# Performance work log

Measured on AMD Instinct MI355X. Metric: run time of the kernel, lower is better.

## Reference

```python
import jax, jax.numpy as jnp
import numpy as np

THRESHOLD = 1.0
SLOPE = 25.0  # snntorch surrogate.fast_sigmoid default

@jax.custom_vjp
def spike_fn(x):
    # heaviside forward, fast_sigmoid surrogate backward
    return (x > 0).astype(x.dtype)

def _spike_fwd(x):
    return spike_fn(x), x

def _spike_bwd(x, g):
    return (g / (SLOPE * jnp.abs(x) + 1.0) ** 2,)

spike_fn.defvjp(_spike_fwd, _spike_bwd)


def setup_inputs() -> dict:
    key = jax.random.key(0)
    ks = jax.random.split(key, 8)
    B, D_IN, H0, H1 = 16384, 512, 1024, 512
    def linear_params(kw, kb, fan_in, fan_out):
        bound = 1.0 / np.sqrt(fan_in)
        w = jax.random.uniform(kw, (fan_out, fan_in), jnp.float32, -bound, bound)
        b = jax.random.uniform(kb, (fan_out,), jnp.float32, -bound, bound)
        return w, b
    w1, b1 = linear_params(ks[0], ks[1], D_IN, H0)
    w2, b2 = linear_params(ks[2], ks[3], H0, H1)
    w3, b3 = linear_params(ks[4], ks[5], H1, 1)
    data = jax.random.normal(ks[6], (B, D_IN), jnp.float32)
    return {"data": data, "w1": w1, "b1": b1, "w2": w2, "b2": b2,
            "w3": w3, "b3": b3, "time_steps": 8}


def reference(data, w1, b1, w2, b2, w3, b3, time_steps):
    # Effective betas: snntorch clamps beta to [0,1]. lif1 beta = units0 (=1024) -> 1.0 (source bug, replicated).
    beta1 = jnp.float32(1.0)
    beta2 = jnp.float32(0.95)
    # data is constant across time, so fc1 output is step-invariant
    cur1 = data @ w1.T + b1                      # [B, H0]
    B, H0 = cur1.shape
    H1 = w2.shape[0]
    mem1_0 = jnp.zeros((B, H0), cur1.dtype)
    mem2_0 = jnp.zeros((B, H1), cur1.dtype)

    def step(carry, _):
        mem1, mem2 = carry
        # snntorch Leaky (reset_mechanism='subtract'): reset detected on OLD mem, detached
        reset1 = jax.lax.stop_gradient((mem1 > THRESHOLD).astype(mem1.dtype))
        mem1 = beta1 * mem1 + cur1 - reset1 * THRESHOLD
        spk1 = spike_fn(mem1 - THRESHOLD)
        cur2 = spk1 @ w2.T + b2                  # [B, H1]
        reset2 = jax.lax.stop_gradient((mem2 > THRESHOLD).astype(mem2.dtype))
        mem2 = beta2 * mem2 + cur2 - reset2 * THRESHOLD
        spk2 = spike_fn(mem2 - THRESHOLD)
        cur3 = spk2 @ w3.T + b3                  # [B, 1]
        return (mem1, mem2), cur3

    _, cur3_seq = jax.lax.scan(step, (mem1_0, mem2_0), None, length=time_steps)
    return jnp.mean(cur3_seq, axis=0)            # [B, 1]
```

## Files before the change

### kernel.cpp

```cpp
#include <hip/hip_runtime.h>
#include <hip/hip_bf16.h>
#include <cstdint>
#include <cstddef>


#define NB 16384
#define DIN 512
#define NH0 1024
#define NH1 512

typedef float f32x4 __attribute__((ext_vector_type(4)));
typedef short bf16x8 __attribute__((ext_vector_type(8)));

#define WS_PAT   0u
#define WS_W2H   19922944u
#define WS_W2M   20971520u
#define WS_W2L   22020096u

__device__ inline uint16_t f2bf(float f) {
    __hip_bfloat16 h = __float2bfloat16(f);
    return *reinterpret_cast<uint16_t*>(&h);
}
__device__ inline float bf2f(uint16_t u) {
    __hip_bfloat16 h = *reinterpret_cast<__hip_bfloat16*>(&u);
    return __bfloat162float(h);
}

__global__ void init_out_kernel(float* __restrict__ out,
                                const float* __restrict__ b3, int n) {
    int i = blockIdx.x * blockDim.x + threadIdx.x;
    if (i < n) out[i] = b3[0];
}

__global__ __launch_bounds__(256) void split3_kernel(
    const float* __restrict__ src, uint16_t* __restrict__ h,
    uint16_t* __restrict__ m, uint16_t* __restrict__ l, int n)
{
    int i = (blockIdx.x * 256 + threadIdx.x) * 4;
    if (i >= n) return;
    float4 f = *(const float4*)(src + i);
    float fv[4] = {f.x, f.y, f.z, f.w};
    uint32_t hw[2], mw[2], lw[2];
    #pragma unroll
    for (int g = 0; g < 2; ++g) {
        uint16_t hh[2], mm[2], ll[2];
        #pragma unroll
        for (int e = 0; e < 2; ++e) {
            float a = fv[2 * g + e];
            uint16_t h0 = f2bf(a);
            float d = __fsub_rn(a, bf2f(h0));
            uint16_t m0 = f2bf(d);
            float e2 = __fsub_rn(d, bf2f(m0));
            uint16_t l0 = f2bf(e2);
            hh[e] = h0; mm[e] = m0; ll[e] = l0;
        }
        hw[g] = (uint32_t)hh[0] | ((uint32_t)hh[1] << 16);
        mw[g] = (uint32_t)mm[0] | ((uint32_t)mm[1] << 16);
        lw[g] = (uint32_t)ll[0] | ((uint32_t)ll[1] << 16);
    }
    *(uint2*)(h + i) = make_uint2(hw[0], hw[1]);
    *(uint2*)(m + i) = make_uint2(mw[0], mw[1]);
    *(uint2*)(l + i) = make_uint2(lw[0], lw[1]);
}

__global__ __launch_bounds__(512, 4) void gemm1_spike_kernel(
    const float* __restrict__ data, const float* __restrict__ w1,
    const float* __restrict__ b1, uint8_t* __restrict__ pat)
{
    __shared__ float As[128][68];
    __shared__ float Bs[128][68];
    const int tid = threadIdx.x;
    const int tx = tid & 31;
    const int ty = tid >> 5;
    const int i0 = blockIdx.x * 128, n0 = blockIdx.y * 128;

    float acc[8][4] = {};

    for (int kb = 0; kb < DIN; kb += 64) {
        #pragma unroll
        for (int rep = 0; rep < 4; ++rep) {
            int idx = tid + rep * 512;
            int row = idx >> 4, c4 = (idx & 15) * 4;
            *(float4*)(&As[row][c4]) =
                *(const float4*)(data + (size_t)(i0 + row) * DIN + kb + c4);
            *(float4*)(&Bs[row][c4]) =
                *(const float4*)(w1 + (size_t)(n0 + row) * DIN + kb + c4);
        }
        __syncthreads();
        #pragma unroll 2
        for (int k4 = 0; k4 < 16; ++k4) {
            float4 a4[8], b4[4];
            #pragma unroll
            for (int ii = 0; ii < 8; ++ii)
                a4[ii] = *(const float4*)(&As[ty + ii * 16][k4 * 4]);
            #pragma unroll
            for (int nn = 0; nn < 4; ++nn)
                b4[nn] = *(const float4*)(&Bs[tx + nn * 32][k4 * 4]);
            #pragma unroll
            for (int ii = 0; ii < 8; ++ii) {
                #pragma unroll
                for (int nn = 0; nn < 4; ++nn) {
                    acc[ii][nn] = fmaf(a4[ii].x, b4[nn].x, acc[ii][nn]);
                    acc[ii][nn] = fmaf(a4[ii].y, b4[nn].y, acc[ii][nn]);
                    acc[ii][nn] = fmaf(a4[ii].z, b4[nn].z, acc[ii][nn]);
                    acc[ii][nn] = fmaf(a4[ii].w, b4[nn].w, acc[ii][nn]);
                }
            }
        }
        __syncthreads();
    }

    #pragma unroll
    for (int ii = 0; ii < 8; ++ii) {
        const int i = i0 + ty + ii * 16;
        #pragma unroll
        for (int nn = 0; nn < 4; ++nn) {
            const int n = n0 + tx + nn * 32;
            float x = __fadd_rn(acc[ii][nn], b1[n]);
            float mem = 0.0f;
            unsigned p = 0;
            #pragma unroll
            for (int t = 0; t < 8; ++t) {
                bool reset = mem > 1.0f;
                float tmp = __fadd_rn(mem, x);
                mem = reset ? __fsub_rn(tmp, 1.0f) : tmp;
                p |= (mem > 1.0f ? 1u : 0u) << t;
            }
            pat[(size_t)(n >> 6) * (NB * 64) + (size_t)i * 64 + (n & 63)] = (uint8_t)p;
        }
    }
}

__global__ __launch_bounds__(256, 2) void gemm2_mfma_kernel(
    const uint8_t* __restrict__ pat,
    const uint16_t* __restrict__ w2h, const uint16_t* __restrict__ w2m,
    const uint16_t* __restrict__ w2l,
    const float* __restrict__ b2, const float* __restrict__ w3,
    float* __restrict__ out)
{
    __shared__ __align__(16) uint16_t Bhi[2][64][72];
    __shared__ __align__(16) uint16_t Bmd[2][64][72];
    __shared__ __align__(16) uint16_t Blo[2][64][72];
    __shared__ __align__(16) uint8_t  Ap[2][64][80];

    const int tid  = threadIdx.x;
    const int lane = tid & 63;
    const int wv   = tid >> 6;
    const int lr   = lane & 15;
    const int lg   = lane >> 4;
    const int i0   = blockIdx.x * 64, n0 = blockIdx.y * 64;

    f32x4 acc[8][4];
    #pragma unroll
    for (int t = 0; t < 8; ++t)
        #pragma unroll
        for (int nf = 0; nf < 4; ++nf)
            acc[t][nf] = (f32x4)(0.0f);

    const int srow = tid >> 2;
    const int scol = (tid & 3) * 16;
    const size_t wbase = (size_t)(n0 + srow) * NH0 + scol;
    const size_t pbase = (size_t)i0 * 64 + (size_t)tid * 16;

    uint4 rh0, rh1, rm0, rm1, rl0, rl1, rp;

    {
        const uint16_t* s1 = w2h + wbase;
        const uint16_t* s2 = w2m + wbase;
        const uint16_t* s3 = w2l + wbase;
        rh0 = *(const uint4*)(s1); rh1 = *(const uint4*)(s1 + 8);
        rm0 = *(const uint4*)(s2); rm1 = *(const uint4*)(s2 + 8);
        rl0 = *(const uint4*)(s3); rl1 = *(const uint4*)(s3 + 8);
        rp  = *(const uint4*)(pat + pbase);
        *(uint4*)(&Bhi[0][srow][scol])     = rh0;
        *(uint4*)(&Bhi[0][srow][scol + 8]) = rh1;
        *(uint4*)(&Bmd[0][srow][scol])     = rm0;
        *(uint4*)(&Bmd[0][srow][scol + 8]) = rm1;
        *(uint4*)(&Blo[0][srow][scol])     = rl0;
        *(uint4*)(&Blo[0][srow][scol + 8]) = rl1;
        *(uint4*)(&Ap[0][srow][scol])      = rp;
    }

    int cur = 0;
    for (int kbi = 0; kbi < 16; ++kbi) {
        __syncthreads();
        if (kbi < 15) {
            const int kb = (kbi + 1) * 64;
            const uint16_t* s1 = w2h + wbase + kb;
            const uint16_t* s2 = w2m + wbase + kb;
            const uint16_t* s3 = w2l + wbase + kb;
            rh0 = *(const uint4*)(s1); rh1 = *(const uint4*)(s1 + 8);
            rm0 = *(const uint4*)(s2); rm1 = *(const uint4*)(s2 + 8);
            rl0 = *(const uint4*)(s3); rl1 = *(const uint4*)(s3 + 8);
            rp  = *(const uint4*)(pat + (size_t)(kbi + 1) * (NB * 64) + pbase);
        }

        #pragma unroll
        for (int s = 0; s < 2; ++s) {
            const int k0 = s * 32;
            bf16x8 bh[4], bm[4], bl[4];
            #pragma unroll
            for (int nf = 0; nf < 4; ++nf) {
                const int col = nf * 16 + lr;
                bh[nf] = *(const bf16x8*)(&Bhi[cur][col][k0 + lg * 8]);
                bm[nf] = *(const bf16x8*)(&Bmd[cur][col][k0 + lg * 8]);
                bl[nf] = *(const bf16x8*)(&Blo[cur][col][k0 + lg * 8]);
            }
            const uint2 p8 = *(const uint2*)(&Ap[cur][wv * 16 + lr][k0 + lg * 8]);
            #pragma unroll
            for (int t = 0; t < 8; ++t) {
                uint32_t y0 = (p8.x >> t) & 0x01010101u;
                uint32_t y1 = (p8.y >> t) & 0x01010101u;
                uint32_t s0 = __builtin_amdgcn_perm(0u, y0, 0x01010000u) | 0x02000200u;
                uint32_t s1x = __builtin_amdgcn_perm(0u, y0, 0x03030202u) | 0x02000200u;
                uint32_t s2x = __builtin_amdgcn_perm(0u, y1, 0x01010000u) | 0x02000200u;
                uint32_t s3x = __builtin_amdgcn_perm(0u, y1, 0x03030202u) | 0x02000200u;
                union { uint4 u; bf16x8 v; } af;
                af.u = make_uint4(__builtin_amdgcn_perm(0u, 0x3F008000u, s0),
                                  __builtin_amdgcn_perm(0u, 0x3F008000u, s1x),
                                  __builtin_amdgcn_perm(0u, 0x3F008000u, s2x),
                                  __builtin_amdgcn_perm(0u, 0x3F008000u, s3x));
                #pragma unroll
                for (int nf = 0; nf < 4; ++nf) {
                    acc[t][nf] = __builtin_amdgcn_mfma_f32_16x16x32_bf16(
                        af.v, bh[nf], acc[t][nf], 0, 0, 0);
                    acc[t][nf] = __builtin_amdgcn_mfma_f32_16x16x32_bf16(
                        af.v, bm[nf], acc[t][nf], 0, 0, 0);
                    acc[t][nf] = __builtin_amdgcn_mfma_f32_16x16x32_bf16(
                        af.v, bl[nf], acc[t][nf], 0, 0, 0);
                }
            }
        }

        if (kbi < 15) {
            const int nb = cur ^ 1;
            *(uint4*)(&Bhi[nb][srow][scol])     = rh0;
            *(uint4*)(&Bhi[nb][srow][scol + 8]) = rh1;
            *(uint4*)(&Bmd[nb][srow][scol])     = rm0;
            *(uint4*)(&Bmd[nb][srow][scol + 8]) = rm1;
            *(uint4*)(&Blo[nb][srow][scol])     = rl0;
            *(uint4*)(&Blo[nb][srow][scol + 8]) = rl1;
            *(uint4*)(&Ap[nb][srow][scol])      = rp;
        }
        cur ^= 1;
    }

    float rowsum[4] = {0.0f, 0.0f, 0.0f, 0.0f};
    #pragma unroll
    for (int nf = 0; nf < 4; ++nf) {
        const int n = n0 + nf * 16 + lr;
        const float b2n = b2[n];
        const float w3n = w3[n];
        #pragma unroll
        for (int r = 0; r < 4; ++r) {
            float mem = 0.0f;
            int pc = 0;
            #pragma unroll
            for (int t = 0; t < 8; ++t) {
                bool reset = mem > 1.0f;
                float x   = __fadd_rn(acc[t][nf][r], b2n);
                float tmp = __fadd_rn(__fmul_rn(0.95f, mem), x);
                mem = reset ? __fsub_rn(tmp, 1.0f) : tmp;
                pc += (mem > 1.0f) ? 1 : 0;
            }
            rowsum[r] = fmaf(w3n, (float)pc, rowsum[r]);
        }
    }
    #pragma unroll
    for (int r = 0; r < 4; ++r) {
        float s = rowsum[r];
        s += __shfl_xor(s, 1);
        s += __shfl_xor(s, 2);
        s += __shfl_xor(s, 4);
        s += __shfl_xor(s, 8);
        if (lr == 0)
            atomicAdd(&out[i0 + wv * 16 + lg * 4 + r], 0.125f * s);
    }
}

extern "C" void kernel_launch(void* const* d_in, const int* in_sizes, int n_in,
                              void* d_out, int out_size, void* d_ws, size_t ws_size,
                              hipStream_t stream) {
    const float* data = (const float*)d_in[0];
    const float* w1   = (const float*)d_in[1];
    const float* b1   = (const float*)d_in[2];
    const float* w2   = (const float*)d_in[3];
    const float* b2   = (const float*)d_in[4];
    const float* w3   = (const float*)d_in[5];
    const float* b3   = (const float*)d_in[6];
    float* out = (float*)d_out;

    char* ws = (char*)d_ws;
    uint8_t*  pat = (uint8_t*)(ws + WS_PAT);
    uint16_t* w2h = (uint16_t*)(ws + WS_W2H);
    uint16_t* w2m = (uint16_t*)(ws + WS_W2M);
    uint16_t* w2l = (uint16_t*)(ws + WS_W2L);

    init_out_kernel<<<(NB + 255) / 256, 256, 0, stream>>>(out, b3, NB);
    split3_kernel<<<(NH1 * NH0 / 4 + 255) / 256, 256, 0, stream>>>(w2, w2h, w2m, w2l, NH1 * NH0);
    gemm1_spike_kernel<<<dim3(NB / 128, NH0 / 128), 512, 0, stream>>>(data, w1, b1, pat);
    gemm2_mfma_kernel<<<dim3(NB / 64, NH1 / 64), 256, 0, stream>>>(pat, w2h, w2m, w2l, b2, w3, out);
}
```

Baseline: 563.1 us.

## Split time steps across two wave groups in gemm2 to halve accumulators

Doubles the gemm2 block to 512 threads: each group of four waves computes four of the eight time steps, so each wave holds half as many accumulators and register pressure drops (launch bounds now 512,3). The first group's accumulators are exchanged through a 64KB shared buffer so the LIF recurrence can run sequentially in one group. Shared-memory staging is flattened into a raw buffer, and each thread loads half as much per tile. The cost is duplicated B-fragment LDS reads and an extra shared-memory pass at the end, and the 64KB of LDS per block may cap residency.

```diff
diff --git a/kernel.cpp b/kernel.cpp
--- a/kernel.cpp
+++ b/kernel.cpp
@@ -131,54 +131,53 @@
     }
 }
 
-__global__ __launch_bounds__(256, 2) void gemm2_mfma_kernel(
+__global__ __launch_bounds__(512, 3) void gemm2_mfma_kernel(
     const uint8_t* __restrict__ pat,
     const uint16_t* __restrict__ w2h, const uint16_t* __restrict__ w2m,
     const uint16_t* __restrict__ w2l,
     const float* __restrict__ b2, const float* __restrict__ w3,
     float* __restrict__ out)
 {
-    __shared__ __align__(16) uint16_t Bhi[2][64][72];
-    __shared__ __align__(16) uint16_t Bmd[2][64][72];
-    __shared__ __align__(16) uint16_t Blo[2][64][72];
-    __shared__ __align__(16) uint8_t  Ap[2][64][80];
+    __shared__ __align__(16) uint8_t lds_raw[65536];
+    uint16_t* Bh_ = (uint16_t*)lds_raw;
+    uint16_t* Bm_ = (uint16_t*)(lds_raw + 18432);
+    uint16_t* Bl_ = (uint16_t*)(lds_raw + 36864);
+    uint8_t*  Ap_ = lds_raw + 55296;
 
     const int tid  = threadIdx.x;
     const int lane = tid & 63;
     const int wv   = tid >> 6;
+    const int tg   = wv >> 2;
+    const int ig   = wv & 3;
     const int lr   = lane & 15;
     const int lg   = lane >> 4;
     const int i0   = blockIdx.x * 64, n0 = blockIdx.y * 64;
 
-    f32x4 acc[8][4];
+    f32x4 acc[4][4];
     #pragma unroll
-    for (int t = 0; t < 8; ++t)
+    for (int tl = 0; tl < 4; ++tl)
         #pragma unroll
         for (int nf = 0; nf < 4; ++nf)
-            acc[t][nf] = (f32x4)(0.0f);
-
-    const int srow = tid >> 2;
-    const int scol = (tid & 3) * 16;
-    const size_t wbase = (size_t)(n0 + srow) * NH0 + scol;
+            acc[tl][nf] = (f32x4)(0.0f);
+
+    const int srow = tid >> 3;
+    const int sc8  = (tid & 7) * 8;
+    const size_t wbase = (size_t)(n0 + srow) * NH0 + sc8;
     const size_t pbase = (size_t)i0 * 64 + (size_t)tid * 16;
 
-    uint4 rh0, rh1, rm0, rm1, rl0, rl1, rp;
+    uint4 rh, rm, rl, rp;
 
     {
-        const uint16_t* s1 = w2h + wbase;
-        const uint16_t* s2 = w2m + wbase;
-        const uint16_t* s3 = w2l + wbase;
-        rh0 = *(const uint4*)(s1); rh1 = *(const uint4*)(s1 + 8);
-        rm0 = *(const uint4*)(s2); rm1 = *(const uint4*)(s2 + 8);
-        rl0 = *(const uint4*)(s3); rl1 = *(const uint4*)(s3 + 8);
-        rp  = *(const uint4*)(pat + pbase);
-        *(uint4*)(&Bhi[0][srow][scol])     = rh0;
-        *(uint4*)(&Bhi[0][srow][scol + 8]) = rh1;
-        *(uint4*)(&Bmd[0][srow][scol])     = rm0;
-        *(uint4*)(&Bmd[0][srow][scol + 8]) = rm1;
-        *(uint4*)(&Blo[0][srow][scol])     = rl0;
-        *(uint4*)(&Blo[0][srow][scol + 8]) = rl1;
-        *(uint4*)(&Ap[0][srow][scol])      = rp;
+        rh = *(const uint4*)(w2h + wbase);
+        rm = *(const uint4*)(w2m + wbase);
+        rl = *(const uint4*)(w2l + wbase);
+        *(uint4*)(Bh_ + srow * 72 + sc8) = rh;
+        *(uint4*)(Bm_ + srow * 72 + sc8) = rm;
+        *(uint4*)(Bl_ + srow * 72 + sc8) = rl;
+        if (tid < 256) {
+            rp = *(const uint4*)(pat + pbase);
+            *(uint4*)(Ap_ + (tid >> 2) * 80 + (tid & 3) * 16) = rp;
+        }
     }
 
     int cur = 0;
@@ -186,13 +185,11 @@
         __syncthreads();
         if (kbi < 15) {
             const int kb = (kbi + 1) * 64;
-            const uint16_t* s1 = w2h + wbase + kb;
-            const uint16_t* s2 = w2m + wbase + kb;
-            const uint16_t* s3 = w2l + wbase + kb;
-            rh0 = *(const uint4*)(s1); rh1 = *(const uint4*)(s1 + 8);
-            rm0 = *(const uint4*)(s2); rm1 = *(const uint4*)(s2 + 8);
-            rl0 = *(const uint4*)(s3); rl1 = *(const uint4*)(s3 + 8);
-            rp  = *(const uint4*)(pat + (size_t)(kbi + 1) * (NB * 64) + pbase);
+            rh = *(const uint4*)(w2h + wbase + kb);
+            rm = *(const uint4*)(w2m + wbase + kb);
+            rl = *(const uint4*)(w2l + wbase + kb);
+            if (tid < 256)
+                rp = *(const uint4*)(pat + (size_t)(kbi + 1) * (NB * 64) + pbase);
         }
 
         #pragma unroll
@@ -202,13 +199,15 @@
             #pragma unroll
             for (int nf = 0; nf < 4; ++nf) {
                 const int col = nf * 16 + lr;
-                bh[nf] = *(const bf16x8*)(&Bhi[cur][col][k0 + lg * 8]);
-                bm[nf] = *(const bf16x8*)(&Bmd[cur][col][k0 + lg * 8]);
-                bl[nf] = *(const bf16x8*)(&Blo[cur][col][k0 + lg * 8]);
-            }
-            const uint2 p8 = *(const uint2*)(&Ap[cur][wv * 16 + lr][k0 + lg * 8]);
-            #pragma unroll
-            for (int t = 0; t < 8; ++t) {
+                bh[nf] = *(const bf16x8*)(Bh_ + (size_t)cur * 4608 + col * 72 + k0 + lg * 8);
+                bm[nf] = *(const bf16x8*)(Bm_ + (size_t)cur * 4608 + col * 72 + k0 + lg * 8);
+                bl[nf] = *(const bf16x8*)(Bl_ + (size_t)cur * 4608 + col * 72 + k0 + lg * 8);
+            }
+            const uint2 p8 = *(const uint2*)(Ap_ + (size_t)cur * 5120 +
+                                             (ig * 16 + lr) * 80 + k0 + lg * 8);
+            #pragma unroll
+            for (int tl = 0; tl < 4; ++tl) {
+                const int t = tg * 4 + tl;
                 uint32_t y0 = (p8.x >> t) & 0x01010101u;
                 uint32_t y1 = (p8.y >> t) & 0x01010101u;
                 uint32_t s0 = __builtin_amdgcn_perm(0u, y0, 0x01010000u) | 0x02000200u;
@@ -222,59 +221,77 @@
                                   __builtin_amdgcn_perm(0u, 0x3F008000u, s3x));
                 #pragma unroll
                 for (int nf = 0; nf < 4; ++nf) {
-                    acc[t][nf] = __builtin_amdgcn_mfma_f32_16x16x32_bf16(
-                        af.v, bh[nf], acc[t][nf], 0, 0, 0);
-                    acc[t][nf] = __builtin_amdgcn_mfma_f32_16x16x32_bf16(
-                        af.v, bm[nf], acc[t][nf], 0, 0, 0);
-                    acc[t][nf] = __builtin_amdgcn_mfma_f32_16x16x32_bf16(
-                        af.v, bl[nf], acc[t][nf], 0, 0, 0);
+                    acc[tl][nf] = __builtin_amdgcn_mfma_f32_16x16x32_bf16(
+                        af.v, bh[nf], acc[tl][nf], 0, 0, 0);
+                    acc[tl][nf] = __builtin_amdgcn_mfma_f32_16x16x32_bf16(
+                        af.v, bm[nf], acc[tl][nf], 0, 0, 0);
+                    acc[tl][nf] = __builtin_amdgcn_mfma_f32_16x16x32_bf16(
+                        af.v, bl[nf], acc[tl][nf], 0, 0, 0);
                 }
             }
         }
 
         if (kbi < 15) {
             const int nb = cur ^ 1;
-            *(uint4*)(&Bhi[nb][srow][scol])     = rh0;
-            *(uint4*)(&Bhi[nb][srow][scol + 8]) = rh1;
-            *(uint4*)(&Bmd[nb][srow][scol])     = rm0;
-            *(uint4*)(&Bmd[nb][srow][scol + 8]) = rm1;
-            *(uint4*)(&Blo[nb][srow][scol])     = rl0;
-            *(uint4*)(&Blo[nb][srow][scol + 8]) = rl1;
-            *(uint4*)(&Ap[nb][srow][scol])      = rp;
+            *(uint4*)(Bh_ + (size_t)nb * 4608 + srow * 72 + sc8) = rh;
+            *(uint4*)(Bm_ + (size_t)nb * 4608 + srow * 72 + sc8) = rm;
+            *(uint4*)(Bl_ + (size_t)nb * 4608 + srow * 72 + sc8) = rl;
+            if (tid < 256)
+                *(uint4*)(Ap_ + (size_t)nb * 5120 + (tid >> 2) * 80 + (tid & 3) * 16) = rp;
         }
         cur ^= 1;
     }
 
-    float rowsum[4] = {0.0f, 0.0f, 0.0f, 0.0f};
-    #pragma unroll
-    for (int nf = 0; nf < 4; ++nf) {
-        const int n = n0 + nf * 16 + lr;
-        const float b2n = b2[n];
-        const float w3n = w3[n];
+    __syncthreads();
+    float* xf = (float*)lds_raw;
+    const int widx = ig * 64 + lane;
+    if (tg == 1) {
+        #pragma unroll
+        for (int tl = 0; tl < 4; ++tl)
+            #pragma unroll
+            for (int nf = 0; nf < 4; ++nf)
+                #pragma unroll
+                for (int r = 0; r < 4; ++r)
+                    xf[(tl * 16 + nf * 4 + r) * 256 + widx] = acc[tl][nf][r];
+    }
+    __syncthreads();
+    if (tg == 0) {
+        float rowsum[4] = {0.0f, 0.0f, 0.0f, 0.0f};
+        #pragma unroll
+        for (int nf = 0; nf < 4; ++nf) {
+            const int n = n0 + nf * 16 + lr;
+            const float b2n = b2[n];
+            const float w3n = w3[n];
+            #pragma unroll
+            for (int r = 0; r < 4; ++r) {
+                float hi4[4];
+                #pragma unroll
+                for (int tl = 0; tl < 4; ++tl)
+                    hi4[tl] = xf[(tl * 16 + nf * 4 + r) * 256 + widx];
+                float mem = 0.0f;
+                int pc = 0;
+                #pragma unroll
+                for (int t = 0; t < 8; ++t) {
+                    bool reset = mem > 1.0f;
+                    float aval = (t < 4) ? acc[t][nf][r] : hi4[t - 4];
+                    float x   = __fadd_rn(aval, b2n);
+                    float tmp = __fadd_rn(__fmul_rn(0.95f, mem), x);
+                    mem = reset ? __fsub_rn(tmp, 1.0f) : tmp;
+                    pc += (mem > 1.0f) ? 1 : 0;
+                }
+                rowsum[r] = fmaf(w3n, (float)pc, rowsum[r]);
+            }
+        }
         #pragma unroll
         for (int r = 0; r < 4; ++r) {
-            float mem = 0.0f;
-            int pc = 0;
-            #pragma unroll
-            for (int t = 0; t < 8; ++t) {
-                bool reset = mem > 1.0f;
-                float x   = __fadd_rn(acc[t][nf][r], b2n);
-                float tmp = __fadd_rn(__fmul_rn(0.95f, mem), x);
-                mem = reset ? __fsub_rn(tmp, 1.0f) : tmp;
-                pc += (mem > 1.0f) ? 1 : 0;
-            }
-            rowsum[r] = fmaf(w3n, (float)pc, rowsum[r]);
-        }
-    }
-    #pragma unroll
-    for (int r = 0; r < 4; ++r) {
-        float s = rowsum[r];
-        s += __shfl_xor(s, 1);
-        s += __shfl_xor(s, 2);
-        s += __shfl_xor(s, 4);
-        s += __shfl_xor(s, 8);
-        if (lr == 0)
-            atomicAdd(&out[i0 + wv * 16 + lg * 4 + r], 0.125f * s);
+            float s = rowsum[r];
+            s += __shfl_xor(s, 1);
+            s += __shfl_xor(s, 2);
+            s += __shfl_xor(s, 4);
+            s += __shfl_xor(s, 8);
+            if (lr == 0)
+                atomicAdd(&out[i0 + ig * 16 + lg * 4 + r], 0.125f * s);
+        }
     }
 }
 
@@ -299,5 +316,5 @@
     init_out_kernel<<<(NB + 255) / 256, 256, 0, stream>>>(out, b3, NB);
     split3_kernel<<<(NH1 * NH0 / 4 + 255) / 256, 256, 0, stream>>>(w2, w2h, w2m, w2l, NH1 * NH0);
     gemm1_spike_kernel<<<dim3(NB / 128, NH0 / 128), 512, 0, stream>>>(data, w1, b1, pat);
-    gemm2_mfma_kernel<<<dim3(NB / 64, NH1 / 64), 256, 0, stream>>>(pat, w2h, w2m, w2l, b2, w3, out);
-}
+    gemm2_mfma_kernel<<<dim3(NB / 64, NH1 / 64), 512, 0, stream>>>(pat, w2h, w2m, w2l, b2, w3, out);
+}
```

Result: no change. 572.9 us (+1.7%).

## Prefetch GEMM1 tiles into registers and use fragment-ordered LDS layout in GEMM2

Applied to the files above, without the earlier changes.

GEMM1 now loads the next K tile from global memory into registers while computing the current one. The intent is to hide global load latency behind the FMA loop, at the cost of 32 extra registers per thread. GEMM2's shared-memory tiles are rearranged into MFMA fragment order, so each lane reads one contiguous 16-byte chunk indexed by lane, which should avoid strided, bank-conflicting LDS reads. The spike-pattern tile is split into two 8-byte writes to match that layout.

```diff
diff --git a/kernel.cpp b/kernel.cpp
--- a/kernel.cpp
+++ b/kernel.cpp
@@ -75,18 +75,34 @@
     const int i0 = blockIdx.x * 128, n0 = blockIdx.y * 128;
 
     float acc[8][4] = {};
+    float4 pa[4], pb[4];
+
+    #pragma unroll
+    for (int rep = 0; rep < 4; ++rep) {
+        int idx = tid + rep * 512;
+        int row = idx >> 4, c4 = (idx & 15) * 4;
+        pa[rep] = *(const float4*)(data + (size_t)(i0 + row) * DIN + c4);
+        pb[rep] = *(const float4*)(w1 + (size_t)(n0 + row) * DIN + c4);
+    }
 
     for (int kb = 0; kb < DIN; kb += 64) {
         #pragma unroll
         for (int rep = 0; rep < 4; ++rep) {
             int idx = tid + rep * 512;
             int row = idx >> 4, c4 = (idx & 15) * 4;
-            *(float4*)(&As[row][c4]) =
-                *(const float4*)(data + (size_t)(i0 + row) * DIN + kb + c4);
-            *(float4*)(&Bs[row][c4]) =
-                *(const float4*)(w1 + (size_t)(n0 + row) * DIN + kb + c4);
+            *(float4*)(&As[row][c4]) = pa[rep];
+            *(float4*)(&Bs[row][c4]) = pb[rep];
         }
         __syncthreads();
+        if (kb + 64 < DIN) {
+            #pragma unroll
+            for (int rep = 0; rep < 4; ++rep) {
+                int idx = tid + rep * 512;
+                int row = idx >> 4, c4 = (idx & 15) * 4;
+                pa[rep] = *(const float4*)(data + (size_t)(i0 + row) * DIN + kb + 64 + c4);
+                pb[rep] = *(const float4*)(w1 + (size_t)(n0 + row) * DIN + kb + 64 + c4);
+            }
+        }
         #pragma unroll 2
         for (int k4 = 0; k4 < 16; ++k4) {
             float4 a4[8], b4[4];
@@ -138,10 +154,10 @@
     const float* __restrict__ b2, const float* __restrict__ w3,
     float* __restrict__ out)
 {
-    __shared__ __align__(16) uint16_t Bhi[2][64][72];
-    __shared__ __align__(16) uint16_t Bmd[2][64][72];
-    __shared__ __align__(16) uint16_t Blo[2][64][72];
-    __shared__ __align__(16) uint8_t  Ap[2][64][80];
+    __shared__ __align__(16) uint16_t Bh_[8192];
+    __shared__ __align__(16) uint16_t Bm_[8192];
+    __shared__ __align__(16) uint16_t Bl_[8192];
+    __shared__ __align__(16) uint8_t  Ap_[8192];
 
     const int tid  = threadIdx.x;
     const int lane = tid & 63;
@@ -161,52 +177,48 @@
     const int scol = (tid & 3) * 16;
     const size_t wbase = (size_t)(n0 + srow) * NH0 + scol;
     const size_t pbase = (size_t)i0 * 64 + (size_t)tid * 16;
+    const int nf_w  = srow >> 4, lr_w = srow & 15;
+    const int ub0 = (((scol >> 5)       * 4 + nf_w) * 64 + ((scol >> 3) & 3)       * 16 + lr_w) * 8;
+    const int ub1 = ((((scol + 8) >> 5) * 4 + nf_w) * 64 + (((scol + 8) >> 3) & 3) * 16 + lr_w) * 8;
 
     uint4 rh0, rh1, rm0, rm1, rl0, rl1, rp;
 
-    {
-        const uint16_t* s1 = w2h + wbase;
-        const uint16_t* s2 = w2m + wbase;
-        const uint16_t* s3 = w2l + wbase;
-        rh0 = *(const uint4*)(s1); rh1 = *(const uint4*)(s1 + 8);
-        rm0 = *(const uint4*)(s2); rm1 = *(const uint4*)(s2 + 8);
-        rl0 = *(const uint4*)(s3); rl1 = *(const uint4*)(s3 + 8);
-        rp  = *(const uint4*)(pat + pbase);
-        *(uint4*)(&Bhi[0][srow][scol])     = rh0;
-        *(uint4*)(&Bhi[0][srow][scol + 8]) = rh1;
-        *(uint4*)(&Bmd[0][srow][scol])     = rm0;
-        *(uint4*)(&Bmd[0][srow][scol + 8]) = rm1;
-        *(uint4*)(&Blo[0][srow][scol])     = rl0;
-        *(uint4*)(&Blo[0][srow][scol + 8]) = rl1;
-        *(uint4*)(&Ap[0][srow][scol])      = rp;
-    }
+#define K2_LOAD(kt) do { \
+        const size_t o = wbase + (size_t)(kt) * 64; \
+        rh0 = *(const uint4*)(w2h + o); rh1 = *(const uint4*)(w2h + o + 8); \
+        rm0 = *(const uint4*)(w2m + o); rm1 = *(const uint4*)(w2m + o + 8); \
+        rl0 = *(const uint4*)(w2l + o); rl1 = *(const uint4*)(w2l + o + 8); \
+        rp  = *(const uint4*)(pat + (size_t)(kt) * (NB * 64) + pbase); \
+    } while (0)
+
+#define K2_WRITE(nb) do { \
+        *(uint4*)(Bh_ + (nb) * 4096 + ub0) = rh0; *(uint4*)(Bh_ + (nb) * 4096 + ub1) = rh1; \
+        *(uint4*)(Bm_ + (nb) * 4096 + ub0) = rm0; *(uint4*)(Bm_ + (nb) * 4096 + ub1) = rm1; \
+        *(uint4*)(Bl_ + (nb) * 4096 + ub0) = rl0; *(uint4*)(Bl_ + (nb) * 4096 + ub1) = rl1; \
+        *(uint2*)(Ap_ + (nb) * 4096 + ub0) = make_uint2(rp.x, rp.y); \
+        *(uint2*)(Ap_ + (nb) * 4096 + ub1) = make_uint2(rp.z, rp.w); \
+    } while (0)
+
+    K2_LOAD(0);
+    K2_WRITE(0);
 
     int cur = 0;
     for (int kbi = 0; kbi < 16; ++kbi) {
         __syncthreads();
-        if (kbi < 15) {
-            const int kb = (kbi + 1) * 64;
-            const uint16_t* s1 = w2h + wbase + kb;
-            const uint16_t* s2 = w2m + wbase + kb;
-            const uint16_t* s3 = w2l + wbase + kb;
-            rh0 = *(const uint4*)(s1); rh1 = *(const uint4*)(s1 + 8);
-            rm0 = *(const uint4*)(s2); rm1 = *(const uint4*)(s2 + 8);
-            rl0 = *(const uint4*)(s3); rl1 = *(const uint4*)(s3 + 8);
-            rp  = *(const uint4*)(pat + (size_t)(kbi + 1) * (NB * 64) + pbase);
-        }
+        if (kbi < 15) K2_LOAD(kbi + 1);
 
         #pragma unroll
         for (int s = 0; s < 2; ++s) {
-            const int k0 = s * 32;
             bf16x8 bh[4], bm[4], bl[4];
             #pragma unroll
             for (int nf = 0; nf < 4; ++nf) {
-                const int col = nf * 16 + lr;
-                bh[nf] = *(const bf16x8*)(&Bhi[cur][col][k0 + lg * 8]);
-                bm[nf] = *(const bf16x8*)(&Bmd[cur][col][k0 + lg * 8]);
-                bl[nf] = *(const bf16x8*)(&Blo[cur][col][k0 + lg * 8]);
-            }
-            const uint2 p8 = *(const uint2*)(&Ap[cur][wv * 16 + lr][k0 + lg * 8]);
+                const int fo = cur * 4096 + ((s * 4 + nf) * 64 + lane) * 8;
+                bh[nf] = *(const bf16x8*)(Bh_ + fo);
+                bm[nf] = *(const bf16x8*)(Bm_ + fo);
+                bl[nf] = *(const bf16x8*)(Bl_ + fo);
+            }
+            const uint2 p8 = *(const uint2*)(Ap_ + cur * 4096 +
+                                             ((s * 4 + wv) * 64 + lane) * 8);
             #pragma unroll
             for (int t = 0; t < 8; ++t) {
                 uint32_t y0 = (p8.x >> t) & 0x01010101u;
@@ -232,16 +244,7 @@
             }
         }
 
-        if (kbi < 15) {
-            const int nb = cur ^ 1;
-            *(uint4*)(&Bhi[nb][srow][scol])     = rh0;
-            *(uint4*)(&Bhi[nb][srow][scol + 8]) = rh1;
-            *(uint4*)(&Bmd[nb][srow][scol])     = rm0;
-            *(uint4*)(&Bmd[nb][srow][scol + 8]) = rm1;
-            *(uint4*)(&Blo[nb][srow][scol])     = rl0;
-            *(uint4*)(&Blo[nb][srow][scol + 8]) = rl1;
-            *(uint4*)(&Ap[nb][srow][scol])      = rp;
-        }
+        if (kbi < 15) K2_WRITE(cur ^ 1);
         cur ^= 1;
     }
 
```

After: 636.0 us. 1.13x slower.
